# Kernel tuning notes

Hardware: AMD Instinct MI355X
Metric: run time of the kernel (lower is better)

The kernel has to match this reference:

```python
import jax, jax.numpy as jnp
from jax import lax
import numpy as np

CODE_DIM = 256
CODE_SIZE = 1024
BETA = 0.25


def _conv2d(x, w, b, stride, pad):
    # x: NCHW, w: OIHW (pytorch Conv2d layout)
    y = lax.conv_general_dilated(x, w, (stride, stride), [(pad, pad), (pad, pad)],
                                 dimension_numbers=('NCHW', 'OIHW', 'NCHW'))
    return y + b[None, :, None, None]


def _conv_transpose2d(x, w, b, stride, pad):
    # w: pytorch ConvTranspose2d layout [in, out, kh, kw]
    kh, kw = w.shape[2], w.shape[3]
    wf = jnp.flip(w, (2, 3)).transpose(1, 0, 2, 3)  # -> OIHW with spatial flip
    y = lax.conv_general_dilated(x, wf, (1, 1),
                                 [(kh - 1 - pad, kh - 1 - pad), (kw - 1 - pad, kw - 1 - pad)],
                                 lhs_dilation=(stride, stride),
                                 dimension_numbers=('NCHW', 'OIHW', 'NCHW'))
    return y + b[None, :, None, None]


def setup_inputs() -> dict:
    key = jax.random.key(0)
    ks = jax.random.split(key, 14)
    f32 = jnp.float32

    def p(k, shape, s=0.05):
        return jax.random.normal(k, shape, f32) * s

    return {
        'x': jax.random.normal(ks[0], (64, 1, 128, 128), f32),
        'enc_w1': p(ks[1], (64, 1, 5, 5)), 'enc_b1': jnp.zeros((64,), f32),
        'enc_w2': p(ks[2], (64, 64, 5, 5)), 'enc_b2': jnp.zeros((64,), f32),
        'enc_w3': p(ks[3], (CODE_DIM, 64, 5, 5)), 'enc_b3': jnp.zeros((CODE_DIM,), f32),
        'codebook': p(ks[4], (CODE_SIZE, CODE_DIM)),
        'dec_w1': p(ks[5], (CODE_DIM, 64, 4, 4)), 'dec_b1': jnp.zeros((64,), f32),
        'dec_w2': p(ks[6], (64, 64, 4, 4)), 'dec_b2': jnp.zeros((64,), f32),
        'dec_w3': p(ks[7], (1, 64, 3, 3)), 'dec_b3': jnp.zeros((1,), f32),
    }


def reference(x, enc_w1, enc_b1, enc_w2, enc_b2, enc_w3, enc_b3, codebook,
              dec_w1, dec_b1, dec_w2, dec_b2, dec_w3, dec_b3):
    # ---- encoder ----
    z = jax.nn.relu(_conv2d(x, enc_w1, enc_b1, 2, 2))
    z = jax.nn.relu(_conv2d(z, enc_w2, enc_b2, 1, 2))
    z = _conv2d(z, enc_w3, enc_b3, 2, 2)  # [B, D, H/4, W/4]

    # ---- quantize (eval mode: no EMA buffer updates) ----
    b, c, h, w = z.shape
    flat = z.transpose(0, 2, 3, 1).reshape(-1, c)  # [BHW, D]
    # ||z||^2 - 2 z.W^T + ||w||^2
    dists = ((flat ** 2).sum(axis=1, keepdims=True)
             - 2.0 * flat @ codebook.T
             + (codebook ** 2).sum(axis=1)[None, :])  # [BHW, K]
    idx = jnp.argmin(dists, axis=1)
    e = codebook[idx].reshape(b, h, w, c).transpose(0, 3, 1, 2)  # [B, D, h, w]
    e_st = lax.stop_gradient(e - z) + z  # straight-through

    # ---- decoder ----
    y = jax.nn.relu(_conv_transpose2d(e_st, dec_w1, dec_b1, 2, 1))
    y = jax.nn.relu(_conv_transpose2d(y, dec_w2, dec_b2, 2, 1))
    x_tilde = jnp.tanh(_conv2d(y, dec_w3, dec_b3, 1, 1))

    diff = jnp.mean((z - lax.stop_gradient(e)) ** 2)
    return x_tilde, diff
```

## Files before the change

kernel.cpp:

```cpp
#include <hip/hip_runtime.h>

typedef _Float16 f16;
typedef _Float16 f16x8 __attribute__((ext_vector_type(8)));
typedef _Float16 f16x4 __attribute__((ext_vector_type(4)));
typedef _Float16 h2 __attribute__((ext_vector_type(2)));
typedef float f32x4 __attribute__((ext_vector_type(4)));
typedef unsigned short u16;
typedef unsigned int u32;

#define DEVI __device__ __forceinline__

DEVI u16 f2h(float f) { f16 h = (f16)f; return __builtin_bit_cast(u16, h); }
DEVI float h2f(u16 u) { f16 h = __builtin_bit_cast(f16, u); return (float)h; }

DEVI int slotf(int P, int c, int r) { return ((c + P) & 3) | (((r + (P >> 2)) & 1) << 2); }

__launch_bounds__(256)
__global__ void prep_wconv_k(const float* __restrict__ src, u16* __restrict__ dst, int nf_sh) {
    int i = blockIdx.x * 256 + threadIdx.x;
    int j = i & 7, lane = (i >> 3) & 63;
    int q = i >> 9;
    int f = q & ((1 << nf_sh) - 1); q >>= nf_sh;
    int pl = q & 1; q >>= 1;
    int icc = q & 1; int tap = q >> 1;
    int oc = (f << 4) + (lane & 15);
    int ic = icc * 32 + ((lane >> 4) << 3) + j;
    float w = src[(oc * 64 + ic) * 25 + tap];
    if (pl == 0) dst[i] = f2h(w);
    else         dst[i] = f2h((w - h2f(f2h(w))) * 4096.f);
}
__launch_bounds__(256)
__global__ void prep_wdec_k(const float* __restrict__ src, u16* __restrict__ dst, int icc_sh) {
    int i = blockIdx.x * 256 + threadIdx.x;
    int j = i & 7, lane = (i >> 3) & 63;
    int f = (i >> 9) & 3;
    int q = i >> 11;
    int icc = q & ((1 << icc_sh) - 1); int tap = q >> icc_sh;
    int oc = (f << 4) + (lane & 15);
    int ic = icc * 32 + ((lane >> 4) << 3) + j;
    dst[i] = f2h(src[(ic * 64 + oc) * 16 + tap]);
}
__launch_bounds__(256)
__global__ void prep_cb_k(const float* __restrict__ cb, u16* __restrict__ dst) {
    int i = blockIdx.x * 256 + threadIdx.x;
    int j = i & 7, lane = (i >> 3) & 63;
    int f = (i >> 9) & 63;
    int q = i >> 15;
    int pl = q & 1; int ks = q >> 1;
    int n = (f << 4) + (lane & 15);
    int k = ks * 32 + ((lane >> 4) << 3) + j;
    float w = cb[n * 256 + k];
    if (pl == 0) dst[i] = f2h(w);
    else         dst[i] = f2h((w - h2f(f2h(w))) * 4096.f);
}
__launch_bounds__(256)
__global__ void prep_cbn_k(const float* __restrict__ cb, float* __restrict__ cbn) {
    int row = blockIdx.x * 256 + threadIdx.x;
    float s = 0.f;
    for (int c = 0; c < 256; c += 4) {
        f32x4 v = *(const f32x4*)&cb[row * 256 + c];
        s = fmaf(v.x, v.x, s); s = fmaf(v.y, v.y, s);
        s = fmaf(v.z, v.z, s); s = fmaf(v.w, v.w, s);
    }
    cbn[row] = s;
}

__launch_bounds__(256)
__global__ void conv1_k(const float* __restrict__ x, const float* __restrict__ w,
                        const float* __restrict__ b, u16* __restrict__ oh, u16* __restrict__ ol) {
    __shared__ float wl[25 * 64];
    __shared__ float bl[64];
    int t = threadIdx.x;
    for (int i = t; i < 1600; i += 256) wl[(i % 25) * 64 + i / 25] = w[i];
    if (t < 64) bl[t] = b[t];
    __syncthreads();
    int p = blockIdx.x * 256 + t;
    int ox = p & 63, oy = (p >> 6) & 63, n = p >> 12;
    f32x4 acc[16];
    #pragma unroll
    for (int c = 0; c < 16; ++c) acc[c] = *(f32x4*)&bl[c * 4];
    for (int dy = 0; dy < 5; ++dy) {
        int iy = 2 * oy - 2 + dy;
        if ((unsigned)iy >= 128u) continue;
        for (int dx = 0; dx < 5; ++dx) {
            int ix = 2 * ox - 2 + dx;
            if ((unsigned)ix >= 128u) continue;
            float v = x[(n * 128 + iy) * 128 + ix];
            const float* wp = &wl[(dy * 5 + dx) * 64];
            #pragma unroll
            for (int c = 0; c < 16; ++c) {
                f32x4 w4 = *(const f32x4*)&wp[c * 4];
                acc[c].x = fmaf(v, w4.x, acc[c].x); acc[c].y = fmaf(v, w4.y, acc[c].y);
                acc[c].z = fmaf(v, w4.z, acc[c].z); acc[c].w = fmaf(v, w4.w, acc[c].w);
            }
        }
    }
    #pragma unroll
    for (int c = 0; c < 16; ++c) {
        ushort4 uh, ul;
        float vv[4] = {acc[c].x, acc[c].y, acc[c].z, acc[c].w};
        u16 rh[4], rl[4];
        #pragma unroll
        for (int k = 0; k < 4; ++k) {
            float v = fmaxf(vv[k], 0.f);
            f16 hh = (f16)v;
            rh[k] = __builtin_bit_cast(u16, hh);
            rl[k] = f2h((v - (float)hh) * 4096.f);
        }
        uh.x = rh[0]; uh.y = rh[1]; uh.z = rh[2]; uh.w = rh[3];
        ul.x = rl[0]; ul.y = rl[1]; ul.z = rl[2]; ul.w = rl[3];
        *(ushort4*)&oh[p * 64 + c * 4] = uh;
        *(ushort4*)&ol[p * 64 + c * 4] = ul;
    }
}

__launch_bounds__(256, 2)
__global__ void conv5w_k(const u16* __restrict__ Ah_g, const u16* __restrict__ Al_g,
                         const u16* __restrict__ wBf, const float* __restrict__ bias,
                         u16* __restrict__ Oh, u16* __restrict__ Ol) {
    constexpr int PATCH = 20;
    constexpr int NPIX = PATCH * PATCH;
    constexpr int PLSZ = (NPIX / 2) * 64;
    __shared__ u16 patch[2 * PLSZ];

    int t = threadIdx.x, l = t & 63, wv = t >> 6, g = l >> 4;
    int qy = wv >> 1, qx = wv & 1;

    int bi = blockIdx.x;
    int wlin = (bi & 7) * ((int)gridDim.x >> 3) + (bi >> 3);
    int txi = wlin & 3; int rest = wlin >> 2;
    int tyi = rest & 3; int n = rest >> 2;
    int iy0 = (tyi << 4) - 2, ix0 = (txi << 4) - 2;

    int ppb[4];
    #pragma unroll
    for (int mi = 0; mi < 4; ++mi) {
        int m = mi * 16 + (l & 15);
        ppb[mi] = ((qy << 3) + (m >> 3)) * PATCH + (qx << 3) + (m & 7);
    }

    f32x4 acc0[4][4], acc1[4][4];
    f32x4 z4 = {0.f, 0.f, 0.f, 0.f};
    #pragma unroll
    for (int mi = 0; mi < 4; ++mi)
        #pragma unroll
        for (int ni = 0; ni < 4; ++ni) { acc0[mi][ni] = z4; acc1[mi][ni] = z4; }

    int tap0 = bi % 25;
    int dy0 = tap0 / 5, dx0 = tap0 - 5 * dy0;
    int tadd0 = dy0 * PATCH + dx0;
    int iccr = bi & 1;
    const size_t tstride = 16 * 512;

    for (int icci = 0; icci < 2; ++icci) {
        int icc = icci ^ iccr;
        __syncthreads();
        for (int i = t; i < NPIX * 8; i += 256) {
            int c = i & 3; int r2 = i >> 2;
            int pl = (r2 >= NPIX); int pp = r2 - pl * NPIX;
            int py = pp / PATCH, px = pp - py * PATCH;
            int iy = iy0 + py, ix = ix0 + px;
            uint4 v = make_uint4(0u, 0u, 0u, 0u);
            if ((unsigned)iy < 64u && (unsigned)ix < 64u)
                v = *(const uint4*)&(pl ? Al_g : Ah_g)[(((n * 64 + iy) * 64 + ix)) * 64 + icc * 32 + c * 8];
            int P = pp >> 1, r = pp & 1;
            int slot = (r << 2) | ((c + P) & 3);
            *(uint4*)&patch[pl * PLSZ + (P << 6) + (slot << 3)] = v;
        }
        __syncthreads();

        const u16* pB = wBf + (size_t)((tap0 * 4 + icc * 2) * 4) * 512 + l * 8;
        int tap = tap0, dx = dx0, tadd = tadd0;
        for (int tapi = 0; tapi < 25; ++tapi) {
            f16x8 Bh[4], Bl[4];
            #pragma unroll
            for (int ni = 0; ni < 4; ++ni) {
                Bh[ni] = *(const f16x8*)&pB[ni * 512];
                Bl[ni] = *(const f16x8*)&pB[(4 + ni) * 512];
            }
            #pragma unroll
            for (int mi = 0; mi < 4; ++mi) {
                int pp = ppb[mi] + tadd;
                int P = pp >> 1, r = pp & 1;
                int offs = (P << 6) + (((r << 2) | ((g + P) & 3)) << 3);
                f16x8 ah = *(const f16x8*)&patch[offs];
                f16x8 al = *(const f16x8*)&patch[PLSZ + offs];
                #pragma unroll
                for (int ni = 0; ni < 4; ++ni) {
                    acc0[mi][ni] = __builtin_amdgcn_mfma_f32_16x16x32_f16(ah, Bh[ni], acc0[mi][ni], 0, 0, 0);
                    acc1[mi][ni] = __builtin_amdgcn_mfma_f32_16x16x32_f16(ah, Bl[ni], acc1[mi][ni], 0, 0, 0);
                    acc1[mi][ni] = __builtin_amdgcn_mfma_f32_16x16x32_f16(al, Bh[ni], acc1[mi][ni], 0, 0, 0);
                }
            }
            pB = (tap == 24) ? (pB - 24 * tstride) : (pB + tstride);
            if (tap == 24) { tap = 0; dx = 0; tadd = 0; }
            else {
                tap++; dx++; tadd++;
                if (dx == 5) { dx = 0; tadd += PATCH - 5; }
            }
        }
    }
    #pragma unroll
    for (int mi = 0; mi < 4; ++mi)
        #pragma unroll
        for (int ni = 0; ni < 4; ++ni) {
            int oc = ni * 16 + (l & 15);
            float bv = bias[oc];
            #pragma unroll
            for (int reg = 0; reg < 4; ++reg) {
                float v = acc0[mi][ni][reg] + acc1[mi][ni][reg] * (1.f / 4096.f) + bv;
                v = fmaxf(v, 0.f);
                int pix = mi * 16 + g * 4 + reg;
                int oy = (tyi << 4) + (qy << 3) + (pix >> 3);
                int ox = (txi << 4) + (qx << 3) + (pix & 7);
                int idx = ((n * 64 + oy) * 64 + ox) * 64 + oc;
                f16 hh = (f16)v;
                Oh[idx] = __builtin_bit_cast(u16, hh);
                Ol[idx] = f2h((v - (float)hh) * 4096.f);
            }
        }
}

__launch_bounds__(512, 4)
__global__ void conv5x_k(const u16* __restrict__ Ah_g, const u16* __restrict__ Al_g,
                         const u16* __restrict__ wBf, const float* __restrict__ bias,
                         u16* __restrict__ Oh, u16* __restrict__ Ol) {
    constexpr int PATCH = 19;
    constexpr int NPIX = PATCH * PATCH;
    constexpr int NPAIR = (NPIX + 1) / 2;
    constexpr int PLSZ = NPAIR * 64;
    __shared__ u16 patch[2 * PLSZ];

    int t = threadIdx.x, l = t & 63, wv = t >> 6, g = l >> 4;
    int wy = wv >> 2, wx = wv & 3;

    int bi = blockIdx.x;
    int wlin = (bi & 7) * ((int)gridDim.x >> 3) + (bi >> 3);
    int txi = wlin & 3; int rest = wlin >> 2;
    int tyi = rest & 3; int n = rest >> 2;
    int iy0 = ((tyi << 3) << 1) - 2, ix0 = ((txi << 3) << 1) - 2;

    int ppb[2];
    #pragma unroll
    for (int mi = 0; mi < 2; ++mi) {
        int m = wy * 32 + mi * 16 + (l & 15);
        ppb[mi] = (2 * (m >> 3)) * PATCH + 2 * (m & 7);
    }

    f32x4 acc0[2][4], acc1[2][4];
    f32x4 z4 = {0.f, 0.f, 0.f, 0.f};
    #pragma unroll
    for (int mi = 0; mi < 2; ++mi)
        #pragma unroll
        for (int ni = 0; ni < 4; ++ni) { acc0[mi][ni] = z4; acc1[mi][ni] = z4; }

    int tap0 = bi % 25;
    int dy0 = tap0 / 5, dx0 = tap0 - 5 * dy0;
    int tadd0 = dy0 * PATCH + dx0;
    int iccr = bi & 1;
    int fg = __builtin_amdgcn_readfirstlane(wx * 4);
    const size_t tstride = (size_t)(4 * 16) * 512;

    for (int icci = 0; icci < 2; ++icci) {
        int icc = icci ^ iccr;
        __syncthreads();
        for (int i = t; i < NPIX * 8; i += 512) {
            int c = i & 3; int r2 = i >> 2;
            int pl = (r2 >= NPIX); int pp = r2 - pl * NPIX;
            int py = pp / PATCH, px = pp - py * PATCH;
            int iy = iy0 + py, ix = ix0 + px;
            uint4 v = make_uint4(0u, 0u, 0u, 0u);
            if ((unsigned)iy < 64u && (unsigned)ix < 64u)
                v = *(const uint4*)&(pl ? Al_g : Ah_g)[(((n * 64 + iy) * 64 + ix)) * 64 + icc * 32 + c * 8];
            int P = pp >> 1, r = pp & 1;
            *(uint4*)&patch[pl * PLSZ + (P << 6) + (slotf(P, c, r) << 3)] = v;
        }
        __syncthreads();

        const u16* pB = wBf + (size_t)((tap0 * 4 + icc * 2) * 16 + fg) * 512 + l * 8;
        int tap = tap0, dx = dx0, tadd = tadd0;
        for (int tapi = 0; tapi < 25; ++tapi) {
            f16x8 ah[2], al[2];
            #pragma unroll
            for (int mi = 0; mi < 2; ++mi) {
                int pp = ppb[mi] + tadd;
                int P = pp >> 1, r = pp & 1;
                int offs = (P << 6) + (slotf(P, g, r) << 3);
                ah[mi] = *(const f16x8*)&patch[offs];
                al[mi] = *(const f16x8*)&patch[PLSZ + offs];
            }
            #pragma unroll
            for (int nc = 0; nc < 2; ++nc) {
                f16x8 Bh0 = *(const f16x8*)&pB[(nc * 2 + 0) * 512];
                f16x8 Bh1 = *(const f16x8*)&pB[(nc * 2 + 1) * 512];
                f16x8 Bl0 = *(const f16x8*)&pB[(16 + nc * 2 + 0) * 512];
                f16x8 Bl1 = *(const f16x8*)&pB[(16 + nc * 2 + 1) * 512];
                #pragma unroll
                for (int mi = 0; mi < 2; ++mi) {
                    int n0 = nc * 2, n1 = nc * 2 + 1;
                    acc0[mi][n0] = __builtin_amdgcn_mfma_f32_16x16x32_f16(ah[mi], Bh0, acc0[mi][n0], 0, 0, 0);
                    acc0[mi][n1] = __builtin_amdgcn_mfma_f32_16x16x32_f16(ah[mi], Bh1, acc0[mi][n1], 0, 0, 0);
                    acc1[mi][n0] = __builtin_amdgcn_mfma_f32_16x16x32_f16(ah[mi], Bl0, acc1[mi][n0], 0, 0, 0);
                    acc1[mi][n0] = __builtin_amdgcn_mfma_f32_16x16x32_f16(al[mi], Bh0, acc1[mi][n0], 0, 0, 0);
                    acc1[mi][n1] = __builtin_amdgcn_mfma_f32_16x16x32_f16(ah[mi], Bl1, acc1[mi][n1], 0, 0, 0);
                    acc1[mi][n1] = __builtin_amdgcn_mfma_f32_16x16x32_f16(al[mi], Bh1, acc1[mi][n1], 0, 0, 0);
                }
            }
            pB = (tap == 24) ? (pB - 24 * tstride) : (pB + tstride);
            if (tap == 24) { tap = 0; dx = 0; tadd = 0; }
            else {
                tap++; dx++; tadd++;
                if (dx == 5) { dx = 0; tadd += PATCH - 5; }
            }
        }
    }
    #pragma unroll
    for (int mi = 0; mi < 2; ++mi)
        #pragma unroll
        for (int ni = 0; ni < 4; ++ni) {
            int oc = (fg + ni) * 16 + (l & 15);
            float bv = bias[oc];
            #pragma unroll
            for (int reg = 0; reg < 4; ++reg) {
                float v = acc0[mi][ni][reg] + acc1[mi][ni][reg] * (1.f / 4096.f) + bv;
                int pix = wy * 32 + mi * 16 + g * 4 + reg;
                int oy = (tyi << 3) + (pix >> 3), ox = (txi << 3) + (pix & 7);
                int idx = ((n * 32 + oy) * 32 + ox) * 256 + oc;
                f16 hh = (f16)v;
                Oh[idx] = __builtin_bit_cast(u16, hh);
                Ol[idx] = f2h((v - (float)hh) * 4096.f);
            }
        }
}

__launch_bounds__(256, 2)
__global__ void quant_k(const u16* __restrict__ zh, const u16* __restrict__ zl,
                        const u16* __restrict__ cbf, const float* __restrict__ cbn,
                        const float* __restrict__ cb, u16* __restrict__ e,
                        float* __restrict__ diff) {
    __shared__ u16 Bbuf[2 * 32 * 512];
    __shared__ float cbn_l[1024];
    __shared__ float zn_l[128];
    __shared__ float bd_l[128];
    __shared__ int   wi_l[128];

    int t = threadIdx.x, l = t & 63, wv = t >> 6, g = l >> 4;
    int bi = blockIdx.x;
    int row0 = bi << 7;

    {
        f32x4 v = *(const f32x4*)&cbn[t * 4];
        *(f32x4*)&cbn_l[t * 4] = v;
    }

    f16x8 Ah[2][8], Al[2][8];
    int rbase = row0 + wv * 32 + (l & 15);
    #pragma unroll
    for (int mi = 0; mi < 2; ++mi)
        #pragma unroll
        for (int ks = 0; ks < 8; ++ks) {
            size_t off = (size_t)(rbase + mi * 16) * 256 + ks * 32 + g * 8;
            Ah[mi][ks] = *(const f16x8*)&zh[off];
            Al[mi][ks] = *(const f16x8*)&zl[off];
        }

    #pragma unroll
    for (int mi = 0; mi < 2; ++mi) {
        float s = 0.f;
        #pragma unroll
        for (int ks = 0; ks < 8; ++ks)
            #pragma unroll
            for (int j = 0; j < 8; ++j) {
                float v = (float)Ah[mi][ks][j] + (float)Al[mi][ks][j] * (1.f / 4096.f);
                s = fmaf(v, v, s);
            }
        s += __shfl_xor(s, 16);
        s += __shfl_xor(s, 32);
        if (g == 0) zn_l[wv * 32 + mi * 16 + (l & 15)] = s;
    }

    float rd[8]; int rc[8];
    #pragma unroll
    for (int s = 0; s < 8; ++s) { rd[s] = 1e30f; rc[s] = 0; }

    int fi = wv * 8;
    {
        int no0 = bi & 31;
        #pragma unroll
        for (int q = 0; q < 8; ++q) {
            int f2 = fi + q;
            int ks = f2 >> 2, pl = (f2 >> 1) & 1, nf = f2 & 1;
            f16x8 v = *(const f16x8*)&cbf[(size_t)(((ks * 2 + pl) * 64) + no0 * 2 + nf) * 512 + l * 8];
            *(uint4*)&Bbuf[(size_t)f2 * 512 + l * 8] = __builtin_bit_cast(uint4, v);
        }
    }
    __syncthreads();

    for (int noi = 0; noi < 32; ++noi) {
        int b = noi & 1;
        int no_cur = (noi + bi) & 31;

        f16x8 pf[8];
        if (noi < 31) {
            int no_n = (noi + 1 + bi) & 31;
            #pragma unroll
            for (int q = 0; q < 8; ++q) {
                int f2 = fi + q;
                int ks = f2 >> 2, pl = (f2 >> 1) & 1, nf = f2 & 1;
                pf[q] = *(const f16x8*)&cbf[(size_t)(((ks * 2 + pl) * 64) + no_n * 2 + nf) * 512 + l * 8];
            }
        }

        f32x4 acc0[2][2], acc1[2][2];
        f32x4 z4 = {0.f, 0.f, 0.f, 0.f};
        #pragma unroll
        for (int mi = 0; mi < 2; ++mi)
            #pragma unroll
            for (int nf = 0; nf < 2; ++nf) { acc0[mi][nf] = z4; acc1[mi][nf] = z4; }

        #pragma unroll
        for (int ks = 0; ks < 8; ++ks) {
            const u16* bb = &Bbuf[(size_t)(b * 32 + ks * 4) * 512 + l * 8];
            f16x8 Bh0 = *(const f16x8*)&bb[0 * 512];
            f16x8 Bh1 = *(const f16x8*)&bb[1 * 512];
            f16x8 Bl0 = *(const f16x8*)&bb[2 * 512];
            f16x8 Bl1 = *(const f16x8*)&bb[3 * 512];
            #pragma unroll
            for (int mi = 0; mi < 2; ++mi) {
                acc0[mi][0] = __builtin_amdgcn_mfma_f32_16x16x32_f16(Ah[mi][ks], Bh0, acc0[mi][0], 0, 0, 0);
                acc0[mi][1] = __builtin_amdgcn_mfma_f32_16x16x32_f16(Ah[mi][ks], Bh1, acc0[mi][1], 0, 0, 0);
                acc1[mi][0] = __builtin_amdgcn_mfma_f32_16x16x32_f16(Ah[mi][ks], Bl0, acc1[mi][0], 0, 0, 0);
                acc1[mi][0] = __builtin_amdgcn_mfma_f32_16x16x32_f16(Al[mi][ks], Bh0, acc1[mi][0], 0, 0, 0);
                acc1[mi][1] = __builtin_amdgcn_mfma_f32_16x16x32_f16(Ah[mi][ks], Bl1, acc1[mi][1], 0, 0, 0);
                acc1[mi][1] = __builtin_amdgcn_mfma_f32_16x16x32_f16(Al[mi][ks], Bh1, acc1[mi][1], 0, 0, 0);
            }
        }

        #pragma unroll
        for (int nf = 0; nf < 2; ++nf) {
            int col = no_cur * 32 + nf * 16 + (l & 15);
            float cn = cbn_l[col];
            #pragma unroll
            for (int mi = 0; mi < 2; ++mi)
                #pragma unroll
                for (int reg = 0; reg < 4; ++reg) {
                    float d = cn - 2.f * (acc0[mi][nf][reg] + acc1[mi][nf][reg] * (1.f / 4096.f));
                    int slot = mi * 4 + reg;
                    if (d < rd[slot] || (d == rd[slot] && col < rc[slot])) { rd[slot] = d; rc[slot] = col; }
                }
        }

        if (noi < 31) {
            #pragma unroll
            for (int q = 0; q < 8; ++q)
                *(uint4*)&Bbuf[(size_t)((1 - b) * 32 + fi + q) * 512 + l * 8] = __builtin_bit_cast(uint4, pf[q]);
        }
        __syncthreads();
    }

    #pragma unroll
    for (int step = 1; step < 16; step <<= 1) {
        #pragma unroll
        for (int s = 0; s < 8; ++s) {
            float od = __shfl_xor(rd[s], step);
            int ocl = __shfl_xor(rc[s], step);
            if (od < rd[s] || (od == rd[s] && ocl < rc[s])) { rd[s] = od; rc[s] = ocl; }
        }
    }
    if ((l & 15) == 0) {
        #pragma unroll
        for (int s = 0; s < 8; ++s) {
            int mi = s >> 2, reg = s & 3;
            int row = wv * 32 + mi * 16 + g * 4 + reg;
            bd_l[row] = rd[s]; wi_l[row] = rc[s];
        }
    }
    __syncthreads();
    if (t < 64) {
        float dval = (zn_l[t] + bd_l[t]) + (zn_l[t + 64] + bd_l[t + 64]);
        #pragma unroll
        for (int step = 1; step < 64; step <<= 1) dval += __shfl_xor(dval, step);
        if (t == 0) atomicAdd(diff, dval * (1.f / 16777216.f));
    }
    __syncthreads();
    for (int r = 0; r < 128; ++r) {
        int wi = wi_l[r];
        e[(size_t)(row0 + r) * 256 + t] = f2h(cb[wi * 256 + t]);
    }
}

template<int ICT>
__launch_bounds__(256)
__global__ void deconv4_k(const u16* __restrict__ in, const u16* __restrict__ wdf,
                          const float* __restrict__ bias, u16* __restrict__ out,
                          int IH, int IW) {
    constexpr int RST = 40;
    constexpr int ICC = ICT / 32;
    constexpr int PLSZ = 81 * RST;
    __shared__ u16 patch[PLSZ];

    int t = threadIdx.x, l = t & 63, wv = t >> 6;
    int wm = wv >> 1, wn = wv & 1, g = l >> 4;

    int bi = blockIdx.x;
    int wlin = (bi & 7) * ((int)gridDim.x >> 3) + (bi >> 3);
    int par = wlin & 3; int ry = par >> 1, rx = par & 1;
    int rest = wlin >> 2;
    int tw = IW >> 3, th = IH >> 3;
    int txi = rest % tw; rest /= tw;
    int tyi = rest % th; int n = rest / th;
    int a0 = tyi << 3, b0 = txi << 3;
    int by0 = ry ? 0 : -1, bx0 = rx ? 0 : -1;
    int OH = IH << 1, OW = IW << 1;

    int pb0[2];
    #pragma unroll
    for (int mi = 0; mi < 2; ++mi) {
        int m = wm * 32 + mi * 16 + (l & 15);
        int pa = m >> 3, pb_ = m & 7;
        pb0[mi] = (pa * 9 + pb_) * RST + g * 8;
    }

    f32x4 acc[2][2];
    f32x4 z4 = {0.f, 0.f, 0.f, 0.f};
    #pragma unroll
    for (int mi = 0; mi < 2; ++mi)
        #pragma unroll
        for (int ni = 0; ni < 2; ++ni) acc[mi][ni] = z4;

    auto ldB = [&](int icc, int tt, f16x8* B) {
        int tty = tt >> 1, ttx = tt & 1;
        int ky = 1 - ry + 2 * tty, kx = 1 - rx + 2 * ttx;
        int tap = ky * 4 + kx;
        #pragma unroll
        for (int ni = 0; ni < 2; ++ni)
            B[ni] = *(const f16x8*)&wdf[(size_t)((tap * ICC + icc) * 4 + wn * 2 + ni) * 512 + l * 8];
    };

    f16x8 B0[2], B1[2];
    {
        int icc0 = (bi >> 2) & (ICC - 1);
        ldB(icc0, bi & 3, B0);
    }

    for (int icci = 0; icci < ICC; ++icci) {
        int icc = (icci + (bi >> 2)) & (ICC - 1);
        __syncthreads();
        for (int i = t; i < 324; i += 256) {
            int c = i & 3; int pp = i >> 2;
            int pr = pp / 9, pc = pp - pr * 9;
            int ar = a0 + by0 + pr, ac = b0 + bx0 + pc;
            uint4 v = make_uint4(0u, 0u, 0u, 0u);
            if ((unsigned)ar < (unsigned)IH && (unsigned)ac < (unsigned)IW)
                v = *(const uint4*)&in[((n * IH + ar) * IW + ac) * ICT + icc * 32 + c * 8];
            *(uint4*)&patch[(pr * 9 + pc) * RST + c * 8] = v;
        }
        __syncthreads();
        #pragma unroll
        for (int tti = 0; tti < 4; ++tti) {
            int tt = (tti + bi) & 3;
            if (!(icci == ICC - 1 && tti == 3)) {
                int nicci = (tti == 3) ? icci + 1 : icci;
                int ntti = (tti == 3) ? 0 : tti + 1;
                int nicc = (nicci + (bi >> 2)) & (ICC - 1);
                ldB(nicc, (ntti + bi) & 3, B1);
            }
            int tty = tt >> 1, ttx = tt & 1;
            int shift = ((1 - tty) * 9 + (1 - ttx)) * RST;
            #pragma unroll
            for (int mi = 0; mi < 2; ++mi) {
                f16x8 a = *(const f16x8*)&patch[pb0[mi] + shift];
                #pragma unroll
                for (int ni = 0; ni < 2; ++ni)
                    acc[mi][ni] = __builtin_amdgcn_mfma_f32_16x16x32_f16(a, B0[ni], acc[mi][ni], 0, 0, 0);
            }
            B0[0] = B1[0]; B0[1] = B1[1];
        }
    }
    #pragma unroll
    for (int mi = 0; mi < 2; ++mi)
        #pragma unroll
        for (int ni = 0; ni < 2; ++ni) {
            int oc = wn * 32 + ni * 16 + (l & 15);
            float bv = bias[oc];
            #pragma unroll
            for (int reg = 0; reg < 4; ++reg) {
                float v = fmaxf(acc[mi][ni][reg] + bv, 0.f);
                int pix = wm * 32 + mi * 16 + g * 4 + reg;
                int oy = ((a0 + (pix >> 3)) << 1) + ry;
                int ox = ((b0 + (pix & 7)) << 1) + rx;
                out[((n * OH + oy) * OW + ox) * 64 + oc] = f2h(v);
            }
        }
}

__launch_bounds__(256)
__global__ void conv3x3_tanh_k(const u16* __restrict__ in, const float* __restrict__ w,
                               const float* __restrict__ b, float* __restrict__ out) {
    __shared__ u16 tile[18 * 18 * 72];
    __shared__ u32 wpk[288];
    int t = threadIdx.x;
    int bi = blockIdx.x;
    int wlin = (bi & 7) * ((int)gridDim.x >> 3) + (bi >> 3);
    int n = wlin >> 6;
    int tile6 = wlin & 63;
    int ty0 = (tile6 >> 3) << 4, tx0 = (tile6 & 7) << 4;

    for (int i = t; i < 288; i += 256) {
        int tap = i >> 5, icp = i & 31;
        h2 p;
        p.x = (f16)w[(2 * icp) * 9 + tap];
        p.y = (f16)w[(2 * icp + 1) * 9 + tap];
        wpk[tap * 32 + icp] = __builtin_bit_cast(u32, p);
    }
    for (int i = t; i < 2592; i += 256) {
        int ch = i & 7, pix = i >> 3;
        int pr = pix / 18, pc = pix - pr * 18;
        int gy = ty0 - 1 + pr, gx = tx0 - 1 + pc;
        uint4 v = make_uint4(0u, 0u, 0u, 0u);
        if ((unsigned)gy < 128u && (unsigned)gx < 128u)
            v = *(const uint4*)&in[(((n << 7) + gy) * 128 + gx) * 64 + ch * 8];
        *(uint4*)&tile[pix * 72 + ch * 8] = v;
    }
    __syncthreads();

    int ty = t >> 4, tx = t & 15;
    float acc = b[0];
    #pragma unroll
    for (int dy = 0; dy < 3; ++dy) {
        #pragma unroll
        for (int dx = 0; dx < 3; ++dx) {
            int base = ((ty + dy) * 18 + (tx + dx)) * 72;
            const u32* wp = &wpk[(dy * 3 + dx) * 32];
            #pragma unroll
            for (int c8 = 0; c8 < 8; ++c8) {
                uint4 v = *(const uint4*)&tile[base + c8 * 8];
                acc = __builtin_amdgcn_fdot2(__builtin_bit_cast(h2, v.x),
                        __builtin_bit_cast(h2, wp[c8 * 4 + 0]), acc, false);
                acc = __builtin_amdgcn_fdot2(__builtin_bit_cast(h2, v.y),
                        __builtin_bit_cast(h2, wp[c8 * 4 + 1]), acc, false);
                acc = __builtin_amdgcn_fdot2(__builtin_bit_cast(h2, v.z),
                        __builtin_bit_cast(h2, wp[c8 * 4 + 2]), acc, false);
                acc = __builtin_amdgcn_fdot2(__builtin_bit_cast(h2, v.w),
                        __builtin_bit_cast(h2, wp[c8 * 4 + 3]), acc, false);
            }
        }
    }
    int oy = ty0 + ty, ox = tx0 + tx;
    out[(n << 14) + (oy << 7) + ox] = tanhf(acc);
}

extern "C" void kernel_launch(void* const* d_in, const int* in_sizes, int n_in,
                              void* d_out, int out_size, void* d_ws, size_t ws_size,
                              hipStream_t stream) {
    (void)in_sizes; (void)n_in; (void)out_size; (void)ws_size;
    const float* x   = (const float*)d_in[0];
    const float* ew1 = (const float*)d_in[1];
    const float* eb1 = (const float*)d_in[2];
    const float* ew2 = (const float*)d_in[3];
    const float* eb2 = (const float*)d_in[4];
    const float* ew3 = (const float*)d_in[5];
    const float* eb3 = (const float*)d_in[6];
    const float* cb  = (const float*)d_in[7];
    const float* dw1 = (const float*)d_in[8];
    const float* db1 = (const float*)d_in[9];
    const float* dw2 = (const float*)d_in[10];
    const float* db2 = (const float*)d_in[11];
    const float* dw3 = (const float*)d_in[12];
    const float* db3 = (const float*)d_in[13];
    float* out = (float*)d_out;

    u16* ws = (u16*)d_ws;
    u16* a1h = ws;             u16* a1l = ws + 16777216;
    u16* zh  = ws;             u16* zl  = ws + 16777216;
    u16* a2h = ws + 33554432;  u16* a2l = ws + 50331648;
    u16* e   = ws + 33554432;
    u16* y1  = ws + 67108864;
    u16* y2  = ws;
    u16* wBf2 = ws + 83886080;
    u16* wBf3 = wBf2 + 204800;
    u16* wd1f = wBf3 + 819200;
    u16* wd2f = wd1f + 262144;
    u16* cbf  = wd2f + 65536;
    float* cbn = (float*)(cbf + 524288);

    hipMemsetAsync(out + 1048576, 0, 4, stream);

    prep_wconv_k<<<800, 256, 0, stream>>>(ew2, wBf2, 2);
    prep_wconv_k<<<3200, 256, 0, stream>>>(ew3, wBf3, 4);
    prep_wdec_k<<<1024, 256, 0, stream>>>(dw1, wd1f, 3);
    prep_wdec_k<<<256, 256, 0, stream>>>(dw2, wd2f, 1);
    prep_cb_k<<<2048, 256, 0, stream>>>(cb, cbf);
    prep_cbn_k<<<4, 256, 0, stream>>>(cb, cbn);

    conv1_k<<<1024, 256, 0, stream>>>(x, ew1, eb1, a1h, a1l);
    conv5w_k<<<1024, 256, 0, stream>>>(a1h, a1l, wBf2, eb2, a2h, a2l);
    conv5x_k<<<1024, 512, 0, stream>>>(a2h, a2l, wBf3, eb3, zh, zl);
    quant_k<<<512, 256, 0, stream>>>(zh, zl, cbf, cbn, cb, e, out + 1048576);
    deconv4_k<256><<<4096, 256, 0, stream>>>(e, wd1f, db1, y1, 32, 32);
    deconv4_k<64><<<16384, 256, 0, stream>>>(y1, wd2f, db2, y2, 64, 64);
    conv3x3_tanh_k<<<4096, 256, 0, stream>>>(y2, dw3, db3, out);
}
```

Before: 652.1 us.

## Merge deconv parity blocks so one block loads a full-channel patch once

Each transposed-conv block now covers all four output parities of an 8x8 input tile. It loads a single 10x10 patch holding every input channel into shared memory once, then loops over parities and channel chunks. The old version had one block per parity and re-staged a 9x9 patch per 32-channel chunk with barriers in between. This removes the redundant global loads and most of the syncs, at the cost of larger shared memory per block (about 53KB for ICT=256), 4x fewer blocks, and possibly lower occupancy.

Result: no change. 644.2 us (-1.2%).

```diff
diff --git a/kernel.cpp b/kernel.cpp
--- a/kernel.cpp
+++ b/kernel.cpp
@@ -491,107 +491,108 @@
 
 template<int ICT>
 __launch_bounds__(256)
-__global__ void deconv4_k(const u16* __restrict__ in, const u16* __restrict__ wdf,
-                          const float* __restrict__ bias, u16* __restrict__ out,
-                          int IH, int IW) {
-    constexpr int RST = 40;
+__global__ void deconv4m_k(const u16* __restrict__ in, const u16* __restrict__ wdf,
+                           const float* __restrict__ bias, u16* __restrict__ out,
+                           int IH, int IW) {
     constexpr int ICC = ICT / 32;
-    constexpr int PLSZ = 81 * RST;
-    __shared__ u16 patch[PLSZ];
+    constexpr int RST = ICT + 8;
+    constexpr int CHK = ICT / 8;
+    __shared__ u16 patch[100 * RST];
 
     int t = threadIdx.x, l = t & 63, wv = t >> 6;
     int wm = wv >> 1, wn = wv & 1, g = l >> 4;
 
     int bi = blockIdx.x;
     int wlin = (bi & 7) * ((int)gridDim.x >> 3) + (bi >> 3);
-    int par = wlin & 3; int ry = par >> 1, rx = par & 1;
-    int rest = wlin >> 2;
     int tw = IW >> 3, th = IH >> 3;
-    int txi = rest % tw; rest /= tw;
+    int txi = wlin % tw; int rest = wlin / tw;
     int tyi = rest % th; int n = rest / th;
     int a0 = tyi << 3, b0 = txi << 3;
-    int by0 = ry ? 0 : -1, bx0 = rx ? 0 : -1;
     int OH = IH << 1, OW = IW << 1;
+
+    for (int i = t; i < 100 * CHK; i += 256) {
+        int c = i % CHK; int pp = i / CHK;
+        int pr = pp / 10, pc = pp - pr * 10;
+        int ar = a0 - 1 + pr, ac = b0 - 1 + pc;
+        uint4 v = make_uint4(0u, 0u, 0u, 0u);
+        if ((unsigned)ar < (unsigned)IH && (unsigned)ac < (unsigned)IW)
+            v = *(const uint4*)&in[((size_t)(n * IH + ar) * IW + ac) * ICT + c * 8];
+        *(uint4*)&patch[(pr * 10 + pc) * RST + c * 8] = v;
+    }
+    __syncthreads();
 
     int pb0[2];
     #pragma unroll
     for (int mi = 0; mi < 2; ++mi) {
         int m = wm * 32 + mi * 16 + (l & 15);
-        int pa = m >> 3, pb_ = m & 7;
-        pb0[mi] = (pa * 9 + pb_) * RST + g * 8;
-    }
-
-    f32x4 acc[2][2];
-    f32x4 z4 = {0.f, 0.f, 0.f, 0.f};
-    #pragma unroll
-    for (int mi = 0; mi < 2; ++mi)
-        #pragma unroll
-        for (int ni = 0; ni < 2; ++ni) acc[mi][ni] = z4;
-
-    auto ldB = [&](int icc, int tt, f16x8* B) {
+        pb0[mi] = ((m >> 3) * 10 + (m & 7)) * RST + g * 8;
+    }
+
+    float bv[2];
+    #pragma unroll
+    for (int ni = 0; ni < 2; ++ni) bv[ni] = bias[wn * 32 + ni * 16 + (l & 15)];
+
+    auto ldB = [&](int par, int icc, int tt, f16x8* B) {
+        int ry = par >> 1, rx = par & 1;
         int tty = tt >> 1, ttx = tt & 1;
-        int ky = 1 - ry + 2 * tty, kx = 1 - rx + 2 * ttx;
-        int tap = ky * 4 + kx;
+        int tap = (1 - ry + 2 * tty) * 4 + (1 - rx + 2 * ttx);
         #pragma unroll
         for (int ni = 0; ni < 2; ++ni)
             B[ni] = *(const f16x8*)&wdf[(size_t)((tap * ICC + icc) * 4 + wn * 2 + ni) * 512 + l * 8];
     };
 
+    constexpr int NSTEP = 4 * ICC * 4;
+    constexpr int ICSH = (ICC == 2) ? 1 : 3;
+
     f16x8 B0[2], B1[2];
-    {
-        int icc0 = (bi >> 2) & (ICC - 1);
-        ldB(icc0, bi & 3, B0);
-    }
-
-    for (int icci = 0; icci < ICC; ++icci) {
-        int icc = (icci + (bi >> 2)) & (ICC - 1);
-        __syncthreads();
-        for (int i = t; i < 324; i += 256) {
-            int c = i & 3; int pp = i >> 2;
-            int pr = pp / 9, pc = pp - pr * 9;
-            int ar = a0 + by0 + pr, ac = b0 + bx0 + pc;
-            uint4 v = make_uint4(0u, 0u, 0u, 0u);
-            if ((unsigned)ar < (unsigned)IH && (unsigned)ac < (unsigned)IW)
-                v = *(const uint4*)&in[((n * IH + ar) * IW + ac) * ICT + icc * 32 + c * 8];
-            *(uint4*)&patch[(pr * 9 + pc) * RST + c * 8] = v;
-        }
-        __syncthreads();
-        #pragma unroll
-        for (int tti = 0; tti < 4; ++tti) {
-            int tt = (tti + bi) & 3;
-            if (!(icci == ICC - 1 && tti == 3)) {
-                int nicci = (tti == 3) ? icci + 1 : icci;
-                int ntti = (tti == 3) ? 0 : tti + 1;
-                int nicc = (nicci + (bi >> 2)) & (ICC - 1);
-                ldB(nicc, (ntti + bi) & 3, B1);
-            }
-            int tty = tt >> 1, ttx = tt & 1;
-            int shift = ((1 - tty) * 9 + (1 - ttx)) * RST;
-            #pragma unroll
-            for (int mi = 0; mi < 2; ++mi) {
-                f16x8 a = *(const f16x8*)&patch[pb0[mi] + shift];
+    ldB(0, 0, 0, B0);
+
+    for (int par = 0; par < 4; ++par) {
+        int ry = par >> 1, rx = par & 1;
+        f32x4 acc[2][2];
+        f32x4 z4 = {0.f, 0.f, 0.f, 0.f};
+        #pragma unroll
+        for (int mi = 0; mi < 2; ++mi)
+            #pragma unroll
+            for (int ni = 0; ni < 2; ++ni) acc[mi][ni] = z4;
+
+        for (int icc = 0; icc < ICC; ++icc) {
+            #pragma unroll
+            for (int tt = 0; tt < 4; ++tt) {
+                int s1 = ((par * ICC + icc) << 2) + tt + 1;
+                if (s1 < NSTEP) {
+                    int tn = s1 & 3;
+                    int in_ = (s1 >> 2) & (ICC - 1);
+                    int pn = s1 >> (2 + ICSH);
+                    ldB(pn, in_, tn, B1);
+                }
+                int tty = tt >> 1, ttx = tt & 1;
+                int shift = ((1 - tty + ry) * 10 + (1 - ttx + rx)) * RST + icc * 32;
                 #pragma unroll
-                for (int ni = 0; ni < 2; ++ni)
-                    acc[mi][ni] = __builtin_amdgcn_mfma_f32_16x16x32_f16(a, B0[ni], acc[mi][ni], 0, 0, 0);
-            }
-            B0[0] = B1[0]; B0[1] = B1[1];
-        }
-    }
-    #pragma unroll
-    for (int mi = 0; mi < 2; ++mi)
-        #pragma unroll
-        for (int ni = 0; ni < 2; ++ni) {
-            int oc = wn * 32 + ni * 16 + (l & 15);
-            float bv = bias[oc];
-            #pragma unroll
-            for (int reg = 0; reg < 4; ++reg) {
-                float v = fmaxf(acc[mi][ni][reg] + bv, 0.f);
-                int pix = wm * 32 + mi * 16 + g * 4 + reg;
-                int oy = ((a0 + (pix >> 3)) << 1) + ry;
-                int ox = ((b0 + (pix & 7)) << 1) + rx;
-                out[((n * OH + oy) * OW + ox) * 64 + oc] = f2h(v);
-            }
-        }
+                for (int mi = 0; mi < 2; ++mi) {
+                    f16x8 a = *(const f16x8*)&patch[pb0[mi] + shift];
+                    #pragma unroll
+                    for (int ni = 0; ni < 2; ++ni)
+                        acc[mi][ni] = __builtin_amdgcn_mfma_f32_16x16x32_f16(a, B0[ni], acc[mi][ni], 0, 0, 0);
+                }
+                B0[0] = B1[0]; B0[1] = B1[1];
+            }
+        }
+        #pragma unroll
+        for (int mi = 0; mi < 2; ++mi)
+            #pragma unroll
+            for (int ni = 0; ni < 2; ++ni) {
+                int oc = wn * 32 + ni * 16 + (l & 15);
+                #pragma unroll
+                for (int reg = 0; reg < 4; ++reg) {
+                    float v = fmaxf(acc[mi][ni][reg] + bv[ni], 0.f);
+                    int pix = wm * 32 + mi * 16 + g * 4 + reg;
+                    int oy = ((a0 + (pix >> 3)) << 1) + ry;
+                    int ox = ((b0 + (pix & 7)) << 1) + rx;
+                    out[((size_t)(n * OH + oy) * OW + ox) * 64 + oc] = f2h(v);
+                }
+            }
+    }
 }
 
 __launch_bounds__(256)
@@ -697,7 +698,7 @@
     conv5w_k<<<1024, 256, 0, stream>>>(a1h, a1l, wBf2, eb2, a2h, a2l);
     conv5x_k<<<1024, 512, 0, stream>>>(a2h, a2l, wBf3, eb3, zh, zl);
     quant_k<<<512, 256, 0, stream>>>(zh, zl, cbf, cbn, cb, e, out + 1048576);
-    deconv4_k<256><<<4096, 256, 0, stream>>>(e, wd1f, db1, y1, 32, 32);
-    deconv4_k<64><<<16384, 256, 0, stream>>>(y1, wd2f, db2, y2, 64, 64);
+    deconv4m_k<256><<<1024, 256, 0, stream>>>(e, wd1f, db1, y1, 32, 32);
+    deconv4m_k<64><<<4096, 256, 0, stream>>>(y1, wd2f, db2, y2, 64, 64);
     conv3x3_tanh_k<<<4096, 256, 0, stream>>>(y2, dw3, db3, out);
 }
```
